# Kernel optimization log

Measured on AMD Instinct MI355X. Metric: run time of the kernel, lower is better.

## Reference

```python
import jax, jax.numpy as jnp
import numpy as np

HIDDEN = 768
HEADS = 12


def setup_inputs() -> dict:
    key = jax.random.key(0)
    ks = jax.random.split(key, 9)
    B, T, C = 2, 4096, HIDDEN
    s = 1.0 / np.sqrt(C)
    x = jax.random.normal(ks[0], (B, T, C), dtype=jnp.float32)
    Wq = jax.random.normal(ks[1], (C, C), dtype=jnp.float32) * s
    bq = jnp.zeros((C,), dtype=jnp.float32)
    Wk = jax.random.normal(ks[2], (C, C), dtype=jnp.float32) * s
    bk = jnp.zeros((C,), dtype=jnp.float32)
    Wv = jax.random.normal(ks[3], (C, C), dtype=jnp.float32) * s
    bv = jnp.zeros((C,), dtype=jnp.float32)
    Wo = jax.random.normal(ks[4], (C, C), dtype=jnp.float32) * s
    bo = jnp.zeros((C,), dtype=jnp.float32)
    return {"x": x, "Wq": Wq, "bq": bq, "Wk": Wk, "bk": bk,
            "Wv": Wv, "bv": bv, "Wo": Wo, "bo": bo}


def reference(x, Wq, bq, Wk, bk, Wv, bv, Wo, bo):
    B, T, C = x.shape
    H = HEADS
    D = C // H
    # projections -> [B, H, T, D]
    def split_heads(y):
        return y.reshape(B, T, H, D).transpose(0, 2, 1, 3)
    q = split_heads(x @ Wq + bq)
    k = split_heads(x @ Wk + bk)
    v = split_heads(x @ Wv + bv)
    # scores [B, H, T, T], scaled by 1/sqrt(D)
    scores = jnp.einsum('bhqd,bhkd->bhqk', q, k) / jnp.sqrt(jnp.asarray(D, x.dtype))
    causal = jnp.tril(jnp.ones((T, T), dtype=bool))
    scores = jnp.where(causal[None, None], scores, jnp.asarray(-jnp.inf, x.dtype))
    weights = jax.nn.softmax(scores, axis=-1)
    # dropout_prob = 0.0 (eval-equivalent), so dropouts are identity
    out = jnp.einsum('bhqk,bhkd->bhqd', weights, v)  # [B,H,T,D]
    out = out.transpose(0, 2, 1, 3).reshape(B, T, C)
    return out @ Wo + bo
```

## Files before the change

kernel.cpp:

```cpp
#include <hip/hip_runtime.h>

typedef unsigned short ushort_t;
typedef __bf16 bf16x8 __attribute__((ext_vector_type(8)));
typedef float f4v __attribute__((ext_vector_type(4)));

#define B_ 2
#define T_ 4096
#define C_ 768
#define H_ 12
#define D_ 64
#define BT_ (B_*T_)

#define XB_SZ   (BT_*C_*2)
#define WT_SZ   (C_*C_*2)
#define QKV_SZ  (BT_*C_*2)
#define WS_XB   0
#define WS_WT   (WS_XB + XB_SZ)
#define WS_Q    (WS_WT + 4*WT_SZ)
#define WS_K    (WS_Q + QKV_SZ)
#define WS_V    (WS_K + QKV_SZ)
#define WS_AO   (WS_V + QKV_SZ)
#define WS_TOTAL (WS_AO + QKV_SZ)

__device__ __forceinline__ ushort_t f2bf(float f) {
    unsigned u = __float_as_uint(f);
    u += 0x7FFFu + ((u >> 16) & 1u);
    return (ushort_t)(u >> 16);
}

__global__ __launch_bounds__(256) void k_convert_x(const float* __restrict__ x,
                                                   ushort_t* __restrict__ xb, int n4) {
    int i = blockIdx.x * 256 + threadIdx.x;
    if (i >= n4) return;
    float4 v = ((const float4*)x)[i];
    ushort4 o;
    o.x = f2bf(v.x); o.y = f2bf(v.y); o.z = f2bf(v.z); o.w = f2bf(v.w);
    ((ushort4*)xb)[i] = o;
}

__global__ __launch_bounds__(256) void k_wt(const float* __restrict__ w0,
                                            const float* __restrict__ w1,
                                            const float* __restrict__ w2,
                                            const float* __restrict__ w3,
                                            ushort_t* __restrict__ wt) {
    __shared__ float tile[32][33];
    int wi = blockIdx.z;
    const float* W = (wi == 0) ? w0 : (wi == 1) ? w1 : (wi == 2) ? w2 : w3;
    ushort_t* out = wt + wi * C_ * C_;
    int k0 = blockIdx.x * 32, n0 = blockIdx.y * 32;
    int tx = threadIdx.x & 31, ty = threadIdx.x >> 5;
#pragma unroll
    for (int i = 0; i < 4; ++i) {
        int kr = ty * 4 + i;
        tile[kr][tx] = W[(k0 + kr) * C_ + n0 + tx];
    }
    __syncthreads();
#pragma unroll
    for (int i = 0; i < 4; ++i) {
        int nr = ty * 4 + i;
        out[(n0 + nr) * C_ + k0 + tx] = f2bf(tile[tx][nr]);
    }
}

__global__ __launch_bounds__(256) void k_gemm_qkv(
    const ushort_t* __restrict__ Xb, const ushort_t* __restrict__ WtAll,
    const float* __restrict__ bq, const float* __restrict__ bk, const float* __restrict__ bv,
    ushort_t* __restrict__ Qo, ushort_t* __restrict__ Ko, ushort_t* __restrict__ Vo) {
    __shared__ ushort_t lsA[128 * 64];
    __shared__ ushort_t lsB[128 * 64];
    char* lsAb = (char*)lsA;
    char* lsBb = (char*)lsB;
    const int z = blockIdx.z;
    const ushort_t* Wt = WtAll + z * C_ * C_;
    const float* bias = (z == 0) ? bq : (z == 1) ? bk : bv;
    const int m0 = blockIdx.x * 128, n0 = blockIdx.y * 128;
    const int tid = threadIdx.x;
    const int w = tid >> 6, lane = tid & 63, lg = lane >> 4, lr = lane & 15;
    const int wm = w >> 1, wn = w & 1;
    f4v acc[4][4] = {};
    for (int ks = 0; ks < 12; ++ks) {
        const int k0 = ks * 64;
        __syncthreads();
#pragma unroll
        for (int i = 0; i < 4; ++i) {
            int s = tid + 256 * i;
            int r = s >> 3, c16 = s & 7;
            uint4 va = *(const uint4*)(Xb + (m0 + r) * C_ + k0 + c16 * 8);
            uint4 vb = *(const uint4*)(Wt + (n0 + r) * C_ + k0 + c16 * 8);
            int off = r * 128 + ((c16 * 16) ^ ((r & 7) << 4));
            *(uint4*)(lsAb + off) = va;
            *(uint4*)(lsBb + off) = vb;
        }
        __syncthreads();
#pragma unroll
        for (int kk = 0; kk < 2; ++kk) {
            bf16x8 af[4], bfr[4];
            const int kb = (kk * 32 + lg * 8) * 2;
#pragma unroll
            for (int i = 0; i < 4; ++i) {
                int ra = wm * 64 + i * 16 + lr;
                af[i] = *(const bf16x8*)(lsAb + ra * 128 + (kb ^ ((ra & 7) << 4)));
                int rb = wn * 64 + i * 16 + lr;
                bfr[i] = *(const bf16x8*)(lsBb + rb * 128 + (kb ^ ((rb & 7) << 4)));
            }
#pragma unroll
            for (int mi = 0; mi < 4; ++mi)
#pragma unroll
                for (int nj = 0; nj < 4; ++nj)
                    acc[mi][nj] = __builtin_amdgcn_mfma_f32_16x16x32_bf16(af[mi], bfr[nj], acc[mi][nj], 0, 0, 0);
        }
    }
    const float scale = (z == 0) ? 0.125f : 1.0f;
    const int mbase = m0 + wm * 64, nbase = n0 + wn * 64;
    if (z < 2) {
        ushort_t* outp = (z == 0) ? Qo : Ko;
#pragma unroll
        for (int mi = 0; mi < 4; ++mi) {
#pragma unroll
            for (int nj = 0; nj < 4; ++nj) {
                int col = nbase + nj * 16 + lr;
                int h = col >> 6, d = col & 63;
                float bv_ = bias[col];
#pragma unroll
                for (int j = 0; j < 4; ++j) {
                    int m = mbase + mi * 16 + lg * 4 + j;
                    int bb = m >> 12, t = m & 4095;
                    outp[((bb * H_ + h) * T_ + t) * D_ + d] = f2bf((acc[mi][nj][j] + bv_) * scale);
                }
            }
        }
    } else {
#pragma unroll
        for (int mi = 0; mi < 4; ++mi) {
            int m0j = mbase + mi * 16 + lg * 4;
            int bb = m0j >> 12, t0 = m0j & 4095;
#pragma unroll
            for (int nj = 0; nj < 4; ++nj) {
                int col = nbase + nj * 16 + lr;
                int h = col >> 6, d = col & 63;
                float bv_ = bias[col];
                ushort4 pk;
                pk.x = f2bf(acc[mi][nj][0] + bv_);
                pk.y = f2bf(acc[mi][nj][1] + bv_);
                pk.z = f2bf(acc[mi][nj][2] + bv_);
                pk.w = f2bf(acc[mi][nj][3] + bv_);
                *(ushort4*)(Vo + ((size_t)(bb * H_ + h) * D_ + d) * T_ + t0) = pk;
            }
        }
    }
}

__global__ __launch_bounds__(256) void k_flash(const ushort_t* __restrict__ Q,
                                               const ushort_t* __restrict__ K,
                                               const ushort_t* __restrict__ Vt,
                                               ushort_t* __restrict__ AO) {
    __shared__ ushort_t lsK[64 * 64];
    __shared__ ushort_t lsV[64 * 64];
    __shared__ ushort_t lsP[4 * 16 * 64];
    char* lsKb = (char*)lsK;
    char* lsVb = (char*)lsV;
    const int idx = blockIdx.x;
    const int qt = 63 - idx / 24;
    const int bh = idx % 24;
    const int b = bh / H_, h = bh % H_;
    const int q0 = qt * 64;
    const int tid = threadIdx.x, w = tid >> 6, lane = tid & 63, lg = lane >> 4, lr = lane & 15;
    char* lsPb = (char*)(lsP + w * 16 * 64);
    const ushort_t* qb = Q + (size_t)bh * T_ * D_;
    const ushort_t* kb = K + (size_t)bh * T_ * D_;
    const ushort_t* vtb = Vt + (size_t)bh * D_ * T_;
    const int wave_qmin = q0 + w * 16;
    bf16x8 aq[2];
#pragma unroll
    for (int kk = 0; kk < 2; ++kk)
        aq[kk] = *(const bf16x8*)(qb + (size_t)(wave_qmin + lr) * D_ + kk * 32 + lg * 8);
    float m_s[4], l_s[4];
    f4v o[4] = {};
#pragma unroll
    for (int j = 0; j < 4; ++j) { m_s[j] = -1e30f; l_s[j] = 0.f; }

    const int ntiles = qt + 1;
    for (int kt = 0; kt < ntiles; ++kt) {
        const int kv0 = kt * 64;
        __syncthreads();
#pragma unroll
        for (int i = 0; i < 2; ++i) {
            int s = tid + 256 * i;
            int r = s >> 3, c = s & 7;
            uint4 vk = *(const uint4*)(kb + (size_t)(kv0 + r) * D_ + c * 8);
            *(uint4*)(lsKb + r * 128 + ((c * 16) ^ ((r & 7) << 4))) = vk;
            uint4 vv = *(const uint4*)(vtb + (size_t)r * T_ + kv0 + c * 8);
            *(uint4*)(lsVb + r * 128 + ((c * 16) ^ ((r & 7) << 4))) = vv;
        }
        __syncthreads();
        f4v sf[4] = {};
#pragma unroll
        for (int kk = 0; kk < 2; ++kk) {
            const int kbyte = (kk * 32 + lg * 8) * 2;
            bf16x8 bk_[4];
#pragma unroll
            for (int nt = 0; nt < 4; ++nt) {
                int rk = nt * 16 + lr;
                bk_[nt] = *(const bf16x8*)(lsKb + rk * 128 + (kbyte ^ ((rk & 7) << 4)));
            }
#pragma unroll
            for (int nt = 0; nt < 4; ++nt)
                sf[nt] = __builtin_amdgcn_mfma_f32_16x16x32_bf16(aq[kk], bk_[nt], sf[nt], 0, 0, 0);
        }
        if (kv0 + 63 > wave_qmin) {
#pragma unroll
            for (int nt = 0; nt < 4; ++nt)
#pragma unroll
                for (int j = 0; j < 4; ++j) {
                    int qg = wave_qmin + lg * 4 + j;
                    int kg = kv0 + nt * 16 + lr;
                    if (kg > qg) sf[nt][j] = -1e30f;
                }
        }
#pragma unroll
        for (int j = 0; j < 4; ++j) {
            float rm = fmaxf(fmaxf(sf[0][j], sf[1][j]), fmaxf(sf[2][j], sf[3][j]));
            rm = fmaxf(rm, __shfl_xor(rm, 1));
            rm = fmaxf(rm, __shfl_xor(rm, 2));
            rm = fmaxf(rm, __shfl_xor(rm, 4));
            rm = fmaxf(rm, __shfl_xor(rm, 8));
            float mo = m_s[j];
            float mn = fmaxf(mo, rm);
            float alpha = __expf(mo - mn);
            float rs = 0.f;
            int prow = lg * 4 + j;
#pragma unroll
            for (int nt = 0; nt < 4; ++nt) {
                float p = __expf(sf[nt][j] - mn);
                rs += p;
                int cbyte = (nt * 16 + lr) * 2;
                *(ushort_t*)(lsPb + prow * 128 + (cbyte ^ ((prow & 7) << 4))) = f2bf(p);
            }
            rs += __shfl_xor(rs, 1);
            rs += __shfl_xor(rs, 2);
            rs += __shfl_xor(rs, 4);
            rs += __shfl_xor(rs, 8);
            l_s[j] = l_s[j] * alpha + rs;
            m_s[j] = mn;
#pragma unroll
            for (int nt = 0; nt < 4; ++nt) o[nt][j] *= alpha;
        }
#pragma unroll
        for (int kk = 0; kk < 2; ++kk) {
            const int kvbyte = (kk * 32 + lg * 8) * 2;
            bf16x8 ap, bv_[4];
            ap = *(const bf16x8*)(lsPb + lr * 128 + (kvbyte ^ ((lr & 7) << 4)));
#pragma unroll
            for (int nt = 0; nt < 4; ++nt) {
                int rd = nt * 16 + lr;
                bv_[nt] = *(const bf16x8*)(lsVb + rd * 128 + (kvbyte ^ ((rd & 7) << 4)));
            }
#pragma unroll
            for (int nt = 0; nt < 4; ++nt)
                o[nt] = __builtin_amdgcn_mfma_f32_16x16x32_bf16(ap, bv_[nt], o[nt], 0, 0, 0);
        }
    }
    ushort_t* aob = AO + (size_t)b * T_ * C_ + h * D_;
#pragma unroll
    for (int j = 0; j < 4; ++j) {
        float inv = 1.f / l_s[j];
        int qg = wave_qmin + lg * 4 + j;
#pragma unroll
        for (int nt = 0; nt < 4; ++nt) {
            int d = nt * 16 + lr;
            aob[(size_t)qg * C_ + d] = f2bf(o[nt][j] * inv);
        }
    }
}

__global__ __launch_bounds__(256) void k_gemm_out(const ushort_t* __restrict__ Ab,
                                                  const ushort_t* __restrict__ Wt,
                                                  const float* __restrict__ bo,
                                                  float* __restrict__ Out) {
    __shared__ ushort_t lsA[128 * 64];
    __shared__ ushort_t lsB[128 * 64];
    char* lsAb = (char*)lsA;
    char* lsBb = (char*)lsB;
    const int m0 = blockIdx.x * 128, n0 = blockIdx.y * 128;
    const int tid = threadIdx.x;
    const int w = tid >> 6, lane = tid & 63, lg = lane >> 4, lr = lane & 15;
    const int wm = w >> 1, wn = w & 1;
    f4v acc[4][4] = {};
    for (int ks = 0; ks < 12; ++ks) {
        const int k0 = ks * 64;
        __syncthreads();
#pragma unroll
        for (int i = 0; i < 4; ++i) {
            int s = tid + 256 * i;
            int r = s >> 3, c16 = s & 7;
            uint4 va = *(const uint4*)(Ab + (m0 + r) * C_ + k0 + c16 * 8);
            uint4 vb = *(const uint4*)(Wt + (n0 + r) * C_ + k0 + c16 * 8);
            int off = r * 128 + ((c16 * 16) ^ ((r & 7) << 4));
            *(uint4*)(lsAb + off) = va;
            *(uint4*)(lsBb + off) = vb;
        }
        __syncthreads();
#pragma unroll
        for (int kk = 0; kk < 2; ++kk) {
            bf16x8 af[4], bfr[4];
            const int kb = (kk * 32 + lg * 8) * 2;
#pragma unroll
            for (int i = 0; i < 4; ++i) {
                int ra = wm * 64 + i * 16 + lr;
                af[i] = *(const bf16x8*)(lsAb + ra * 128 + (kb ^ ((ra & 7) << 4)));
                int rb = wn * 64 + i * 16 + lr;
                bfr[i] = *(const bf16x8*)(lsBb + rb * 128 + (kb ^ ((rb & 7) << 4)));
            }
#pragma unroll
            for (int mi = 0; mi < 4; ++mi)
#pragma unroll
                for (int nj = 0; nj < 4; ++nj)
                    acc[mi][nj] = __builtin_amdgcn_mfma_f32_16x16x32_bf16(af[mi], bfr[nj], acc[mi][nj], 0, 0, 0);
        }
    }
    const int mbase = m0 + wm * 64, nbase = n0 + wn * 64;
#pragma unroll
    for (int mi = 0; mi < 4; ++mi) {
#pragma unroll
        for (int nj = 0; nj < 4; ++nj) {
            int col = nbase + nj * 16 + lr;
            float bv_ = bo[col];
#pragma unroll
            for (int j = 0; j < 4; ++j) {
                int m = mbase + mi * 16 + lg * 4 + j;
                Out[(size_t)m * C_ + col] = acc[mi][nj][j] + bv_;
            }
        }
    }
}

extern "C" void kernel_launch(void* const* d_in, const int* in_sizes, int n_in,
                              void* d_out, int out_size, void* d_ws, size_t ws_size,
                              hipStream_t stream) {
    const float* x  = (const float*)d_in[0];
    const float* Wq = (const float*)d_in[1];
    const float* bq = (const float*)d_in[2];
    const float* Wk = (const float*)d_in[3];
    const float* bk = (const float*)d_in[4];
    const float* Wv = (const float*)d_in[5];
    const float* bv = (const float*)d_in[6];
    const float* Wo = (const float*)d_in[7];
    const float* bo = (const float*)d_in[8];
    float* out = (float*)d_out;
    char* ws = (char*)d_ws;
    if (ws_size < (size_t)WS_TOTAL) return;

    ushort_t* Xb = (ushort_t*)(ws + WS_XB);
    ushort_t* Wt = (ushort_t*)(ws + WS_WT);
    ushort_t* Qb = (ushort_t*)(ws + WS_Q);
    ushort_t* Kb = (ushort_t*)(ws + WS_K);
    ushort_t* Vb = (ushort_t*)(ws + WS_V);
    ushort_t* Ao = (ushort_t*)(ws + WS_AO);

    k_convert_x<<<dim3(BT_ * C_ / 4 / 256), 256, 0, stream>>>(x, Xb, BT_ * C_ / 4);
    k_wt<<<dim3(24, 24, 4), 256, 0, stream>>>(Wq, Wk, Wv, Wo, Wt);
    k_gemm_qkv<<<dim3(64, 6, 3), 256, 0, stream>>>(Xb, Wt, bq, bk, bv, Qb, Kb, Vb);
    k_flash<<<dim3(64 * 24), 256, 0, stream>>>(Qb, Kb, Vb, Ao);
    k_gemm_out<<<dim3(64, 6), 256, 0, stream>>>(Ao, Wt + 3 * C_ * C_, bo, out);
}
```

Before: 334.0 us.

## Use direct global-to-LDS loads, pair causal q-tiles per block, exp2 softmax

Replaces register-staged global loads with global_load_lds direct-to-LDS transfers in both GEMMs and the flash kernel, applying the XOR swizzle on the source column. The flash kernel now processes two complementary query tiles per block (qt and 63-qt) so every block does equal causal work, and the launch grid is halved. Q is prescaled by log2(e)/sqrt(D) so the softmax can use exp2f, and MFMA sections are wrapped in s_setprio. Risks include the LDS layout of direct loads not matching the swizzled reads, and fewer blocks reducing occupancy.

```diff
diff --git a/kernel.cpp b/kernel.cpp
--- a/kernel.cpp
+++ b/kernel.cpp
@@ -22,10 +22,18 @@
 #define WS_AO   (WS_V + QKV_SZ)
 #define WS_TOTAL (WS_AO + QKV_SZ)
 
+#define QSCALE  0.18033688f
+
 __device__ __forceinline__ ushort_t f2bf(float f) {
     unsigned u = __float_as_uint(f);
     u += 0x7FFFu + ((u >> 16) & 1u);
     return (ushort_t)(u >> 16);
+}
+
+__device__ __forceinline__ void gload16(const void* gsrc, void* ldst) {
+    __builtin_amdgcn_global_load_lds(
+        (const __attribute__((address_space(1))) unsigned int*)gsrc,
+        (__attribute__((address_space(3))) unsigned int*)ldst, 16, 0, 0);
 }
 
 __global__ __launch_bounds__(256) void k_convert_x(const float* __restrict__ x,
@@ -84,12 +92,9 @@
 #pragma unroll
         for (int i = 0; i < 4; ++i) {
             int s = tid + 256 * i;
-            int r = s >> 3, c16 = s & 7;
-            uint4 va = *(const uint4*)(Xb + (m0 + r) * C_ + k0 + c16 * 8);
-            uint4 vb = *(const uint4*)(Wt + (n0 + r) * C_ + k0 + c16 * 8);
-            int off = r * 128 + ((c16 * 16) ^ ((r & 7) << 4));
-            *(uint4*)(lsAb + off) = va;
-            *(uint4*)(lsBb + off) = vb;
+            int r = s >> 3, cs = (s & 7) ^ (r & 7);
+            gload16(Xb + (m0 + r) * C_ + k0 + cs * 8, lsAb + i * 4096 + w * 1024);
+            gload16(Wt + (n0 + r) * C_ + k0 + cs * 8, lsBb + i * 4096 + w * 1024);
         }
         __syncthreads();
 #pragma unroll
@@ -110,7 +115,7 @@
                     acc[mi][nj] = __builtin_amdgcn_mfma_f32_16x16x32_bf16(af[mi], bfr[nj], acc[mi][nj], 0, 0, 0);
         }
     }
-    const float scale = (z == 0) ? 0.125f : 1.0f;
+    const float scale = (z == 0) ? QSCALE : 1.0f;
     const int mbase = m0 + wm * 64, nbase = n0 + wn * 64;
     if (z < 2) {
         ushort_t* outp = (z == 0) ? Qo : Ko;
@@ -160,115 +165,121 @@
     char* lsKb = (char*)lsK;
     char* lsVb = (char*)lsV;
     const int idx = blockIdx.x;
-    const int qt = 63 - idx / 24;
+    const int pi = idx / 24;
     const int bh = idx % 24;
     const int b = bh / H_, h = bh % H_;
-    const int q0 = qt * 64;
     const int tid = threadIdx.x, w = tid >> 6, lane = tid & 63, lg = lane >> 4, lr = lane & 15;
     char* lsPb = (char*)(lsP + w * 16 * 64);
     const ushort_t* qb = Q + (size_t)bh * T_ * D_;
     const ushort_t* kb = K + (size_t)bh * T_ * D_;
     const ushort_t* vtb = Vt + (size_t)bh * D_ * T_;
-    const int wave_qmin = q0 + w * 16;
-    bf16x8 aq[2];
-#pragma unroll
-    for (int kk = 0; kk < 2; ++kk)
-        aq[kk] = *(const bf16x8*)(qb + (size_t)(wave_qmin + lr) * D_ + kk * 32 + lg * 8);
-    float m_s[4], l_s[4];
-    f4v o[4] = {};
-#pragma unroll
-    for (int j = 0; j < 4; ++j) { m_s[j] = -1e30f; l_s[j] = 0.f; }
-
-    const int ntiles = qt + 1;
-    for (int kt = 0; kt < ntiles; ++kt) {
-        const int kv0 = kt * 64;
-        __syncthreads();
-#pragma unroll
-        for (int i = 0; i < 2; ++i) {
-            int s = tid + 256 * i;
-            int r = s >> 3, c = s & 7;
-            uint4 vk = *(const uint4*)(kb + (size_t)(kv0 + r) * D_ + c * 8);
-            *(uint4*)(lsKb + r * 128 + ((c * 16) ^ ((r & 7) << 4))) = vk;
-            uint4 vv = *(const uint4*)(vtb + (size_t)r * T_ + kv0 + c * 8);
-            *(uint4*)(lsVb + r * 128 + ((c * 16) ^ ((r & 7) << 4))) = vv;
-        }
-        __syncthreads();
-        f4v sf[4] = {};
-#pragma unroll
-        for (int kk = 0; kk < 2; ++kk) {
-            const int kbyte = (kk * 32 + lg * 8) * 2;
-            bf16x8 bk_[4];
+    ushort_t* aob = AO + (size_t)b * T_ * C_ + h * D_;
+
+    for (int half = 0; half < 2; ++half) {
+        const int qt = half ? pi : (63 - pi);
+        const int q0 = qt * 64;
+        const int wave_qmin = q0 + w * 16;
+        bf16x8 aq[2];
+#pragma unroll
+        for (int kk = 0; kk < 2; ++kk)
+            aq[kk] = *(const bf16x8*)(qb + (size_t)(wave_qmin + lr) * D_ + kk * 32 + lg * 8);
+        float m_s[4], l_s[4];
+        f4v o[4] = {};
+#pragma unroll
+        for (int j = 0; j < 4; ++j) { m_s[j] = -1e30f; l_s[j] = 0.f; }
+
+        const int ntiles = qt + 1;
+        for (int kt = 0; kt < ntiles; ++kt) {
+            const int kv0 = kt * 64;
+            __syncthreads();
+#pragma unroll
+            for (int i = 0; i < 2; ++i) {
+                int s = tid + 256 * i;
+                int r = s >> 3, cs = (s & 7) ^ (r & 7);
+                gload16(kb + (size_t)(kv0 + r) * D_ + cs * 8, lsKb + i * 4096 + w * 1024);
+                gload16(vtb + (size_t)r * T_ + kv0 + cs * 8, lsVb + i * 4096 + w * 1024);
+            }
+            __syncthreads();
+            f4v sf[4] = {};
+#pragma unroll
+            for (int kk = 0; kk < 2; ++kk) {
+                const int kbyte = (kk * 32 + lg * 8) * 2;
+                bf16x8 bk_[4];
+#pragma unroll
+                for (int nt = 0; nt < 4; ++nt) {
+                    int rk = nt * 16 + lr;
+                    bk_[nt] = *(const bf16x8*)(lsKb + rk * 128 + (kbyte ^ ((rk & 7) << 4)));
+                }
+                __builtin_amdgcn_s_setprio(1);
+#pragma unroll
+                for (int nt = 0; nt < 4; ++nt)
+                    sf[nt] = __builtin_amdgcn_mfma_f32_16x16x32_bf16(aq[kk], bk_[nt], sf[nt], 0, 0, 0);
+                __builtin_amdgcn_s_setprio(0);
+            }
+            if (kv0 + 63 > wave_qmin) {
+#pragma unroll
+                for (int nt = 0; nt < 4; ++nt)
+#pragma unroll
+                    for (int j = 0; j < 4; ++j) {
+                        int qg = wave_qmin + lg * 4 + j;
+                        int kg = kv0 + nt * 16 + lr;
+                        if (kg > qg) sf[nt][j] = -1e30f;
+                    }
+            }
+#pragma unroll
+            for (int j = 0; j < 4; ++j) {
+                float rm = fmaxf(fmaxf(sf[0][j], sf[1][j]), fmaxf(sf[2][j], sf[3][j]));
+                rm = fmaxf(rm, __shfl_xor(rm, 1));
+                rm = fmaxf(rm, __shfl_xor(rm, 2));
+                rm = fmaxf(rm, __shfl_xor(rm, 4));
+                rm = fmaxf(rm, __shfl_xor(rm, 8));
+                float mo = m_s[j];
+                float mn = fmaxf(mo, rm);
+                float alpha = exp2f(mo - mn);
+                float rs = 0.f;
+                int prow = lg * 4 + j;
+#pragma unroll
+                for (int nt = 0; nt < 4; ++nt) {
+                    float p = exp2f(sf[nt][j] - mn);
+                    rs += p;
+                    int cbyte = (nt * 16 + lr) * 2;
+                    *(ushort_t*)(lsPb + prow * 128 + (cbyte ^ ((prow & 7) << 4))) = f2bf(p);
+                }
+                rs += __shfl_xor(rs, 1);
+                rs += __shfl_xor(rs, 2);
+                rs += __shfl_xor(rs, 4);
+                rs += __shfl_xor(rs, 8);
+                l_s[j] = l_s[j] * alpha + rs;
+                m_s[j] = mn;
+#pragma unroll
+                for (int nt = 0; nt < 4; ++nt) o[nt][j] *= alpha;
+            }
+#pragma unroll
+            for (int kk = 0; kk < 2; ++kk) {
+                const int kvbyte = (kk * 32 + lg * 8) * 2;
+                bf16x8 ap, bv_[4];
+                ap = *(const bf16x8*)(lsPb + lr * 128 + (kvbyte ^ ((lr & 7) << 4)));
+#pragma unroll
+                for (int nt = 0; nt < 4; ++nt) {
+                    int rd = nt * 16 + lr;
+                    bv_[nt] = *(const bf16x8*)(lsVb + rd * 128 + (kvbyte ^ ((rd & 7) << 4)));
+                }
+                __builtin_amdgcn_s_setprio(1);
+#pragma unroll
+                for (int nt = 0; nt < 4; ++nt)
+                    o[nt] = __builtin_amdgcn_mfma_f32_16x16x32_bf16(ap, bv_[nt], o[nt], 0, 0, 0);
+                __builtin_amdgcn_s_setprio(0);
+            }
+        }
+#pragma unroll
+        for (int j = 0; j < 4; ++j) {
+            float inv = 1.f / l_s[j];
+            int qg = wave_qmin + lg * 4 + j;
 #pragma unroll
             for (int nt = 0; nt < 4; ++nt) {
-                int rk = nt * 16 + lr;
-                bk_[nt] = *(const bf16x8*)(lsKb + rk * 128 + (kbyte ^ ((rk & 7) << 4)));
-            }
-#pragma unroll
-            for (int nt = 0; nt < 4; ++nt)
-                sf[nt] = __builtin_amdgcn_mfma_f32_16x16x32_bf16(aq[kk], bk_[nt], sf[nt], 0, 0, 0);
-        }
-        if (kv0 + 63 > wave_qmin) {
-#pragma unroll
-            for (int nt = 0; nt < 4; ++nt)
-#pragma unroll
-                for (int j = 0; j < 4; ++j) {
-                    int qg = wave_qmin + lg * 4 + j;
-                    int kg = kv0 + nt * 16 + lr;
-                    if (kg > qg) sf[nt][j] = -1e30f;
-                }
-        }
-#pragma unroll
-        for (int j = 0; j < 4; ++j) {
-            float rm = fmaxf(fmaxf(sf[0][j], sf[1][j]), fmaxf(sf[2][j], sf[3][j]));
-            rm = fmaxf(rm, __shfl_xor(rm, 1));
-            rm = fmaxf(rm, __shfl_xor(rm, 2));
-            rm = fmaxf(rm, __shfl_xor(rm, 4));
-            rm = fmaxf(rm, __shfl_xor(rm, 8));
-            float mo = m_s[j];
-            float mn = fmaxf(mo, rm);
-            float alpha = __expf(mo - mn);
-            float rs = 0.f;
-            int prow = lg * 4 + j;
-#pragma unroll
-            for (int nt = 0; nt < 4; ++nt) {
-                float p = __expf(sf[nt][j] - mn);
-                rs += p;
-                int cbyte = (nt * 16 + lr) * 2;
-                *(ushort_t*)(lsPb + prow * 128 + (cbyte ^ ((prow & 7) << 4))) = f2bf(p);
-            }
-            rs += __shfl_xor(rs, 1);
-            rs += __shfl_xor(rs, 2);
-            rs += __shfl_xor(rs, 4);
-            rs += __shfl_xor(rs, 8);
-            l_s[j] = l_s[j] * alpha + rs;
-            m_s[j] = mn;
-#pragma unroll
-            for (int nt = 0; nt < 4; ++nt) o[nt][j] *= alpha;
-        }
-#pragma unroll
-        for (int kk = 0; kk < 2; ++kk) {
-            const int kvbyte = (kk * 32 + lg * 8) * 2;
-            bf16x8 ap, bv_[4];
-            ap = *(const bf16x8*)(lsPb + lr * 128 + (kvbyte ^ ((lr & 7) << 4)));
-#pragma unroll
-            for (int nt = 0; nt < 4; ++nt) {
-                int rd = nt * 16 + lr;
-                bv_[nt] = *(const bf16x8*)(lsVb + rd * 128 + (kvbyte ^ ((rd & 7) << 4)));
-            }
-#pragma unroll
-            for (int nt = 0; nt < 4; ++nt)
-                o[nt] = __builtin_amdgcn_mfma_f32_16x16x32_bf16(ap, bv_[nt], o[nt], 0, 0, 0);
-        }
-    }
-    ushort_t* aob = AO + (size_t)b * T_ * C_ + h * D_;
-#pragma unroll
-    for (int j = 0; j < 4; ++j) {
-        float inv = 1.f / l_s[j];
-        int qg = wave_qmin + lg * 4 + j;
-#pragma unroll
-        for (int nt = 0; nt < 4; ++nt) {
-            int d = nt * 16 + lr;
-            aob[(size_t)qg * C_ + d] = f2bf(o[nt][j] * inv);
+                int d = nt * 16 + lr;
+                aob[(size_t)qg * C_ + d] = f2bf(o[nt][j] * inv);
+            }
         }
     }
 }
@@ -292,12 +303,9 @@
 #pragma unroll
         for (int i = 0; i < 4; ++i) {
             int s = tid + 256 * i;
-            int r = s >> 3, c16 = s & 7;
-            uint4 va = *(const uint4*)(Ab + (m0 + r) * C_ + k0 + c16 * 8);
-            uint4 vb = *(const uint4*)(Wt + (n0 + r) * C_ + k0 + c16 * 8);
-            int off = r * 128 + ((c16 * 16) ^ ((r & 7) << 4));
-            *(uint4*)(lsAb + off) = va;
-            *(uint4*)(lsBb + off) = vb;
+            int r = s >> 3, cs = (s & 7) ^ (r & 7);
+            gload16(Ab + (m0 + r) * C_ + k0 + cs * 8, lsAb + i * 4096 + w * 1024);
+            gload16(Wt + (n0 + r) * C_ + k0 + cs * 8, lsBb + i * 4096 + w * 1024);
         }
         __syncthreads();
 #pragma unroll
@@ -360,6 +368,6 @@
     k_convert_x<<<dim3(BT_ * C_ / 4 / 256), 256, 0, stream>>>(x, Xb, BT_ * C_ / 4);
     k_wt<<<dim3(24, 24, 4), 256, 0, stream>>>(Wq, Wk, Wv, Wo, Wt);
     k_gemm_qkv<<<dim3(64, 6, 3), 256, 0, stream>>>(Xb, Wt, bq, bk, bv, Qb, Kb, Vb);
-    k_flash<<<dim3(64 * 24), 256, 0, stream>>>(Qb, Kb, Vb, Ao);
+    k_flash<<<dim3(32 * 24), 256, 0, stream>>>(Qb, Kb, Vb, Ao);
     k_gemm_out<<<dim3(64, 6), 256, 0, stream>>>(Ao, Wt + 3 * C_ * C_, bo, out);
 }
```

Result: slower. 342.9 us (+2.7%).
